# Performance work log

Measured on AMD Instinct MI355X. Metric: run time of the kernel, lower is better.

Reference implementation:

```python
import jax, jax.numpy as jnp
import numpy as np
from jax import lax

# Quantization bit-widths per the module: QuantAct(16) on input,
# QuantConv2d(precision[0]=8), QuantAct(precision[0]+3=11) after relu1,
# QuantLinear(precision[1]=8).
INPUT_BIT = 16
CONV_W_BIT = 8
RELU_BIT = 11
DENSE_W_BIT = 8
EPS = 1e-8


def round_ste(x):
    # straight-through estimator rounding (HAWQ SymmetricQuantFunction)
    return x + lax.stop_gradient(jnp.round(x) - x)


def quant_act(x, bit):
    """Per-tensor symmetric dynamic activation quantization (HAWQ QuantAct).
    Returns fake-quantized x and its scaling factor."""
    n = 2 ** (bit - 1) - 1
    scale = lax.stop_gradient(jnp.maximum(jnp.max(jnp.abs(x)), EPS) / n)
    x_q = jnp.clip(round_ste(x / scale), -n, n) * scale
    return x_q, scale


def quant_weight(w, bit):
    """Per-output-channel symmetric weight quantization. w: [out, ...].
    Returns integer-valued weights and per-channel scale [out]."""
    n = 2 ** (bit - 1) - 1
    absmax = jnp.max(jnp.abs(w.reshape(w.shape[0], -1)), axis=1)
    sf = lax.stop_gradient(jnp.maximum(absmax, EPS) / n)
    bshape = (w.shape[0],) + (1,) * (w.ndim - 1)
    w_int = jnp.clip(round_ste(w / sf.reshape(bshape)), -n, n)
    return w_int, sf


def quant_conv2d(x, p_sf, w, b, bit, stride, pad):
    w_int, w_sf = quant_weight(w, bit)          # [O,I,kh,kw], [O]
    x_int = x / p_sf                            # integer-valued activations
    out_int = lax.conv_general_dilated(
        x_int, w_int, window_strides=(stride, stride),
        padding=((pad, pad), (pad, pad)),
        dimension_numbers=("NCHW", "OIHW", "NCHW"))
    bias_sf = p_sf * w_sf                       # [O]
    b_int = round_ste(b / bias_sf)
    out = (out_int + b_int[None, :, None, None]) * bias_sf[None, :, None, None]
    return out, w_sf


def quant_linear(x, p_sf, w, b, bit):
    w_int, w_sf = quant_weight(w, bit)          # [O,I], [O]
    x_int = x / p_sf
    bias_sf = p_sf * w_sf                       # [O]
    b_int = round_ste(b / bias_sf)
    out = (jnp.einsum("bi,oi->bo", x_int, w_int) + b_int[None, :]) * bias_sf[None, :]
    return out


def setup_inputs() -> dict:
    key = jax.random.key(0)
    k1, k2, k3, k4, k5 = jax.random.split(key, 5)
    B, Cin, H, W = 256, 3, 64, 64
    Cout, K = 64, 3
    Fin, Fout = Cout * 32 * 32, 256  # stride-2 conv -> 32x32 spatial
    x = jax.random.normal(k1, (B, Cin, H, W), dtype=jnp.float32)
    conv_w = jax.random.normal(k2, (Cout, Cin, K, K), dtype=jnp.float32) * 0.1
    conv_b = jax.random.normal(k3, (Cout,), dtype=jnp.float32) * 0.01
    dense_w = jax.random.normal(k4, (Fout, Fin), dtype=jnp.float32) * 0.02
    dense_b = jax.random.normal(k5, (Fout,), dtype=jnp.float32) * 0.01
    return {"x": x, "conv_w": conv_w, "conv_b": conv_b,
            "dense_w": dense_w, "dense_b": dense_b}


def reference(x, conv_w, conv_b, dense_w, dense_b):
    # x, p_sf = quant_input(x)
    xq, p_sf = quant_act(x, INPUT_BIT)
    # x, w_sf = conv(x, p_sf)
    h, w_sf = quant_conv2d(xq, p_sf, conv_w, conv_b, CONV_W_BIT, stride=2, pad=1)
    # relu1
    h = jax.nn.relu(h)
    # x, p_sf = quant_relu(x, p_sf, w_sf)  (requantize at relu_bit)
    h, p_sf = quant_act(h, RELU_BIT)
    # flatten
    h = h.reshape(h.shape[0], -1)
    # relu2(enc_dense(x, p_sf))
    out = jax.nn.relu(quant_linear(h, p_sf, dense_w, dense_b, DENSE_W_BIT))
    return out
```

## Files before the change

### kernel.cpp

```cpp
#include <hip/hip_runtime.h>
#include <hip/hip_fp16.h>
#include <cstdint>

#define B_   256
#define CIN  3
#define HW_  64
#define COUT 64
#define FIN  65536
#define FOUT 256

#define ACC_F    0
#define SC_F     65536
#define XPART_F  65552
#define WPART_F  66064
#define CSF_F    67088
#define CWINT_F  67152
#define H16_BYTE (512*1024)
#define WQ_BYTE  (H16_BYTE + 256ll*FIN*2)
#define REP_BYTE (WQ_BYTE + 256ll*FIN)
#define WS_NEED  (REP_BYTE + 64ll*B_*FOUT*4)

typedef _Float16 half8  __attribute__((ext_vector_type(8)));
typedef float    floatx4 __attribute__((ext_vector_type(4)));
typedef unsigned short u16;
typedef unsigned int uint_;

__device__ inline float blockMax(float v) {
    #pragma unroll
    for (int off = 32; off; off >>= 1) v = fmaxf(v, __shfl_down(v, off));
    __shared__ float sm[8];
    const int lane = threadIdx.x & 63, w = threadIdx.x >> 6;
    if (lane == 0) sm[w] = v;
    __syncthreads();
    float m = sm[0];
    const int nw = blockDim.x >> 6;
    for (int i = 1; i < nw; i++) m = fmaxf(m, sm[i]);
    return m;
}

__global__ __launch_bounds__(256) void k_stats(const float* __restrict__ x,
                                               const float* __restrict__ dw,
                                               const float* __restrict__ cw,
                                               float* __restrict__ ws) {
    const int b = blockIdx.x;
    const int t = threadIdx.x;
    if (b < 512) {
        const float4* x4 = (const float4*)x;
        float m = 0.f;
        for (int i = b * 256 + t; i < (B_ * CIN * HW_ * HW_) / 4; i += 512 * 256) {
            float4 v = x4[i];
            m = fmaxf(m, fmaxf(fmaxf(fabsf(v.x), fabsf(v.y)), fmaxf(fabsf(v.z), fabsf(v.w))));
        }
        float bm = blockMax(m);
        if (t == 0) ws[XPART_F + b] = bm;
    } else if (b < 1536) {
        const int b2 = b - 512;
        const int row = b2 >> 2, q = b2 & 3;
        const float4* r = (const float4*)(dw + (size_t)row * FIN) + q * 4096;
        float m = 0.f;
        for (int i = t; i < 4096; i += 256) {
            float4 v = r[i];
            m = fmaxf(m, fmaxf(fmaxf(fabsf(v.x), fabsf(v.y)), fmaxf(fabsf(v.z), fabsf(v.w))));
        }
        float bm = blockMax(m);
        if (t == 0) ws[WPART_F + b2] = bm;
    } else if (b == 1536) {
        if (t == 64) ((unsigned*)ws)[SC_F + 1] = 0u;
        if (t < 64) {
            const int o = t;
            float wv[27];
            float m = 0.f;
            #pragma unroll
            for (int i = 0; i < 27; i++) { wv[i] = cw[o * 27 + i]; m = fmaxf(m, fabsf(wv[i])); }
            const float sf = fmaxf(m, 1e-8f) / 127.0f;
            #pragma unroll
            for (int i = 0; i < 27; i++)
                ws[CWINT_F + o * 27 + i] = fminf(127.f, fmaxf(-127.f, rintf(wv[i] / sf)));
            ws[CSF_F + o] = sf;
        }
    } else {
        ws[ACC_F + (b - 1537) * 256 + t] = 0.f;
    }
}

__global__ __launch_bounds__(256) void k_conv(const float* __restrict__ x,
                                              const float* __restrict__ dw,
                                              const float* __restrict__ cb,
                                              const float* __restrict__ ws,
                                              u16* __restrict__ h16,
                                              signed char* __restrict__ wq,
                                              unsigned* __restrict__ maxh) {
    const int t = threadIdx.x;

    __shared__ float s_bsf[64], s_bint[64];
    __shared__ float xt[27 * 68];

    float pm = fmaxf(ws[XPART_F + t], ws[XPART_F + 256 + t]);
    pm = blockMax(pm);
    const float p_sf = fmaxf(pm, 1e-8f) / 32767.0f;
    const float inv_p = 1.0f / p_sf;
    if (t < 64) {
        const float bsf = p_sf * ws[CSF_F + t];
        s_bsf[t]  = bsf;
        s_bint[t] = rintf(cb[t] / bsf);
    }

    const int b   = blockIdx.x >> 3;
    const int oyt = (blockIdx.x & 7) * 4;
    const float* xb = x + (size_t)b * (CIN * HW_ * HW_);

    for (int i = t; i < 432; i += 256) {
        const int lrow = i >> 4, c4 = i & 15;
        const int ci = lrow / 9, lr = lrow - ci * 9;
        const int iy = 2 * oyt - 1 + lr;
        float4 v = make_float4(0.f, 0.f, 0.f, 0.f);
        if ((unsigned)iy < 64u) v = *(const float4*)(xb + (ci * HW_ + iy) * HW_ + c4 * 4);
        float* d = &xt[lrow * 68 + 1 + c4 * 4];
        d[0] = rintf(v.x * inv_p);
        d[1] = rintf(v.y * inv_p);
        d[2] = rintf(v.z * inv_p);
        d[3] = rintf(v.w * inv_p);
    }
    if (t < 27) xt[t * 68] = 0.f;
    else if (t < 54) xt[(t - 27) * 68 + 65] = 0.f;
    __syncthreads();

    const int ox = t & 31;
    const int ch = __builtin_amdgcn_readfirstlane((t >> 6) & 1);
    const int dy = ((t >> 7) << 1) + ((t >> 5) & 1);
    const int oy = oyt + dy;

    float xs[27];
    #pragma unroll
    for (int ci = 0; ci < 3; ci++)
        #pragma unroll
        for (int ky = 0; ky < 3; ky++) {
            const float* rowp = &xt[(ci * 9 + 2 * dy + ky) * 68 + 2 * ox];
            float a0 = rowp[0], a1 = rowp[1], a2 = rowp[2];
            asm volatile("" : "+v"(a0), "+v"(a1), "+v"(a2));
            xs[ci * 9 + ky * 3 + 0] = a0;
            xs[ci * 9 + ky * 3 + 1] = a1;
            xs[ci * 9 + ky * 3 + 2] = a2;
        }

    const float* wr = ws + CWINT_F + ch * (32 * 27);
    float mx = 0.f;
    u16* outp = h16 + (size_t)b * FIN + (size_t)ch * 32 * 1024 + oy * 32 + ox;

#define EMIT(cc, aa) { const int co_ = ch * 32 + (cc); \
    float h_ = ((aa) + s_bint[co_]) * s_bsf[co_]; \
    h_ = fmaxf(h_, 0.f); mx = fmaxf(mx, h_); \
    outp[(size_t)(cc) * 1024] = __half_as_ushort(__float2half(h_)); }

    float wA[27], wB[27];
    #pragma unroll
    for (int k = 0; k < 27; k++) wA[k] = wr[k];
    #pragma unroll
    for (int c = 0; c < 32; c += 2) {
        #pragma unroll
        for (int k = 0; k < 27; k++) wB[k] = wr[(c + 1) * 27 + k];
        float a = 0.f;
        #pragma unroll
        for (int k = 0; k < 27; k++) a = fmaf(xs[k], wA[k], a);
        EMIT(c, a);
        if (c + 2 < 32) {
            #pragma unroll
            for (int k = 0; k < 27; k++) wA[k] = wr[(c + 2) * 27 + k];
        }
        float a2 = 0.f;
        #pragma unroll
        for (int k = 0; k < 27; k++) a2 = fmaf(xs[k], wB[k], a2);
        EMIT(c + 1, a2);
    }
#undef EMIT
    float bm = blockMax(mx);
    if (t == 0) atomicMax(maxh, __float_as_uint(bm));

    {
        const int row = blockIdx.x >> 3;
        const int e8  = blockIdx.x & 7;
        const float* wp = ws + WPART_F + row * 4;
        const float am = fmaxf(fmaxf(wp[0], wp[1]), fmaxf(wp[2], wp[3]));
        const float inv = 127.0f / fmaxf(am, 1e-8f);
        const float4* r4 = (const float4*)(dw + (size_t)row * FIN) + e8 * 2048;
        uint_* wrow = (uint_*)(wq + (size_t)row * FIN) + e8 * 2048;
        for (int i = t; i < 2048; i += 256) {
            float4 v = r4[i];
            int q0 = __float2int_rn(v.x * inv);
            int q1 = __float2int_rn(v.y * inv);
            int q2 = __float2int_rn(v.z * inv);
            int q3 = __float2int_rn(v.w * inv);
            wrow[i] = (uint_)(q0 & 255) | ((uint_)(q1 & 255) << 8) |
                      ((uint_)(q2 & 255) << 16) | ((uint_)(q3 & 255) << 24);
        }
    }
}

__device__ __forceinline__ half8 cvt_b8(uint_ lo, uint_ hi) {
    half8 h;
    h[0] = (_Float16)(float)(int)(signed char)(lo);
    h[1] = (_Float16)(float)(int)(signed char)(lo >> 8);
    h[2] = (_Float16)(float)(int)(signed char)(lo >> 16);
    h[3] = (_Float16)(float)(int)(signed char)(lo >> 24);
    h[4] = (_Float16)(float)(int)(signed char)(hi);
    h[5] = (_Float16)(float)(int)(signed char)(hi >> 8);
    h[6] = (_Float16)(float)(int)(signed char)(hi >> 16);
    h[7] = (_Float16)(float)(int)(signed char)(hi >> 24);
    return h;
}

#define GEMM_BODY(EPILOGUE) \
    __shared__ __align__(16) _Float16 As[128][72]; \
    __shared__ __align__(16) _Float16 Bs[128][72]; \
    const int tid = threadIdx.x; \
    const int tm  = (blockIdx.x >> 1) * 128; \
    const int tn  = (blockIdx.x & 1) * 128; \
    const int k0  = blockIdx.y * 1024; \
    const float max_h  = __uint_as_float(((const unsigned*)ws)[SC_F + 1]); \
    const float p2     = fmaxf(max_h, 1e-8f) / 1023.0f; \
    const float inv_p2 = 1.0f / p2; \
    floatx4 acc[4][4]; \
    const floatx4 zz = {0.f, 0.f, 0.f, 0.f}; \
    _Pragma("unroll") \
    for (int i = 0; i < 4; i++) _Pragma("unroll") \
        for (int j = 0; j < 4; j++) acc[i][j] = zz; \
    const int wv = tid >> 6, lane = tid & 63; \
    const int wm = (wv >> 1) * 64, wn = (wv & 1) * 64; \
    const int lm = lane & 15, quad = lane >> 4; \
    const int arow = tid >> 3, acol = tid & 7; \
    const int brow = tid >> 1, bq   = (tid & 1) * 32; \
    const u16* abase = h16 + (size_t)(tm + arow) * FIN + k0 + acol * 8; \
    const signed char* bbase = wq + (size_t)(tn + brow) * FIN + k0 + bq; \
    half8 a0[4], a1[4], a2[4]; \
    uint4 b0[2], b1[2], b2[2]; \
    LOADA(a0, 0); LOADB(b0, 0); \
    LOADA(a1, 1); LOADB(b1, 1); \
    LOADA(a2, 2); LOADB(b2, 2); \
    PHASE(a0, b0, 0); \
    for (int it = 0; it < 5; ++it) { \
        PHASE(a1, b1, 3 * it + 1); \
        PHASE(a2, b2, 3 * it + 2); \
        PHASE(a0, b0, 3 * it + 3); \
    } \
    EPILOGUE

#define LOADA(dst, kk) { _Pragma("unroll") \
    for (int r = 0; r < 4; r++) \
        dst[r] = *(const half8*)(abase + (size_t)r * 32 * FIN + (kk) * 64); }
#define LOADB(dst, kk) { const uint4* p_ = (const uint4*)(bbase + (kk) * 64); \
    dst[0] = p_[0]; dst[1] = p_[1]; }
#define STAGEA(src) { _Pragma("unroll") \
    for (int r = 0; r < 4; r++) { half8 qv; _Pragma("unroll") \
        for (int j = 0; j < 8; j++) { float f_ = (float)src[r][j]; \
            qv[j] = (_Float16)fminf(1023.f, rintf(f_ * inv_p2)); } \
        *(half8*)&As[arow + r * 32][acol * 8] = qv; } }
#define STAGEB(src) { _Pragma("unroll") \
    for (int u = 0; u < 2; u++) { uint4 wd_ = src[u]; \
        *(half8*)&Bs[brow][bq + u * 16 + 0] = cvt_b8(wd_.x, wd_.y); \
        *(half8*)&Bs[brow][bq + u * 16 + 8] = cvt_b8(wd_.z, wd_.w); } }
#define BARRIER() do { asm volatile("s_waitcnt lgkmcnt(0)" ::: "memory"); \
    __builtin_amdgcn_s_barrier(); } while (0)
#define MFMA_PHASE() { _Pragma("unroll") \
    for (int ks = 0; ks < 2; ks++) { half8 af[4], bf[4]; _Pragma("unroll") \
        for (int mi = 0; mi < 4; mi++) \
            af[mi] = *(const half8*)&As[wm + mi * 16 + lm][ks * 32 + quad * 8]; \
        _Pragma("unroll") \
        for (int ni = 0; ni < 4; ni++) \
            bf[ni] = *(const half8*)&Bs[wn + ni * 16 + lm][ks * 32 + quad * 8]; \
        _Pragma("unroll") \
        for (int mi = 0; mi < 4; mi++) _Pragma("unroll") \
            for (int ni = 0; ni < 4; ni++) \
                acc[mi][ni] = __builtin_amdgcn_mfma_f32_16x16x32_f16(af[mi], bf[ni], acc[mi][ni], 0, 0, 0); } }
#define PHASE(As_, Bs_, kk) { \
    STAGEA(As_); STAGEB(Bs_); \
    if ((kk) + 3 < 16) { LOADA(As_, (kk) + 3); LOADB(Bs_, (kk) + 3); } \
    BARRIER(); \
    MFMA_PHASE(); \
    BARRIER(); }

__global__ __launch_bounds__(256) void k_gemm_rep(const u16* __restrict__ h16,
                                                  const signed char* __restrict__ wq,
                                                  const float* __restrict__ ws,
                                                  float* __restrict__ rep) {
    GEMM_BODY({
        float* rp = rep + (size_t)blockIdx.y * (B_ * FOUT);
        _Pragma("unroll")
        for (int mi = 0; mi < 4; mi++) _Pragma("unroll")
            for (int ni = 0; ni < 4; ni++) _Pragma("unroll")
                for (int r = 0; r < 4; r++) {
                    const int row = tm + wm + mi * 16 + quad * 4 + r;
                    const int col = tn + wn + ni * 16 + lm;
                    rp[row * FOUT + col] = acc[mi][ni][r];
                }
    })
}

__global__ __launch_bounds__(256) void k_gemm_atm(const u16* __restrict__ h16,
                                                  const signed char* __restrict__ wq,
                                                  const float* __restrict__ ws,
                                                  float* __restrict__ accb) {
    GEMM_BODY({
        _Pragma("unroll")
        for (int mi = 0; mi < 4; mi++) _Pragma("unroll")
            for (int ni = 0; ni < 4; ni++) _Pragma("unroll")
                for (int r = 0; r < 4; r++) {
                    const int row = tm + wm + mi * 16 + quad * 4 + r;
                    const int col = tn + wn + ni * 16 + lm;
                    atomicAdd(accb + row * FOUT + col, acc[mi][ni][r]);
                }
    })
}
#undef LOADA
#undef LOADB
#undef STAGEA
#undef STAGEB
#undef BARRIER
#undef MFMA_PHASE
#undef PHASE
#undef GEMM_BODY

__global__ void k_epi_rep(const float* __restrict__ rep, const float* __restrict__ db,
                          const float* __restrict__ ws, float* __restrict__ out) {
    const int idx = blockIdx.x * 256 + threadIdx.x;
    float s0 = 0.f, s1 = 0.f, s2 = 0.f, s3 = 0.f;
    #pragma unroll
    for (int r = 0; r < 64; r += 4) {
        s0 += rep[(size_t)(r + 0) * (B_ * FOUT) + idx];
        s1 += rep[(size_t)(r + 1) * (B_ * FOUT) + idx];
        s2 += rep[(size_t)(r + 2) * (B_ * FOUT) + idx];
        s3 += rep[(size_t)(r + 3) * (B_ * FOUT) + idx];
    }
    const float sum = (s0 + s1) + (s2 + s3);
    const int n = idx & 255;
    const float max_h = __uint_as_float(((const unsigned*)ws)[SC_F + 1]);
    const float p2 = fmaxf(max_h, 1e-8f) / 1023.0f;
    const float* wp = ws + WPART_F + (size_t)n * 4;
    const float am = fmaxf(fmaxf(fmaxf(wp[0], wp[1]), fmaxf(wp[2], wp[3])), 1e-8f);
    const float bsf = p2 * (am / 127.0f);
    const float bint = rintf(db[n] / bsf);
    out[idx] = fmaxf(0.f, (sum + bint) * bsf);
}

__global__ void k_epi_atm(const float* __restrict__ accb, const float* __restrict__ db,
                          const float* __restrict__ ws, float* __restrict__ out) {
    const int idx = blockIdx.x * 256 + threadIdx.x;
    const int n = idx & 255;
    const float max_h = __uint_as_float(((const unsigned*)ws)[SC_F + 1]);
    const float p2 = fmaxf(max_h, 1e-8f) / 1023.0f;
    const float* wp = ws + WPART_F + (size_t)n * 4;
    const float am = fmaxf(fmaxf(fmaxf(wp[0], wp[1]), fmaxf(wp[2], wp[3])), 1e-8f);
    const float bsf = p2 * (am / 127.0f);
    const float bint = rintf(db[n] / bsf);
    out[idx] = fmaxf(0.f, (accb[idx] + bint) * bsf);
}

extern "C" void kernel_launch(void* const* d_in, const int* in_sizes, int n_in,
                              void* d_out, int out_size, void* d_ws, size_t ws_size,
                              hipStream_t stream) {
    (void)in_sizes; (void)n_in; (void)out_size;
    const float* x  = (const float*)d_in[0];
    const float* cw = (const float*)d_in[1];
    const float* cb = (const float*)d_in[2];
    const float* dw = (const float*)d_in[3];
    const float* db = (const float*)d_in[4];
    float* out = (float*)d_out;
    float* ws  = (float*)d_ws;
    u16* h16   = (u16*)((char*)d_ws + H16_BYTE);
    signed char* wq = (signed char*)d_ws + WQ_BYTE;
    float* rep  = (float*)((char*)d_ws + REP_BYTE);
    float* accb = ws + ACC_F;
    unsigned* maxh = (unsigned*)ws + SC_F + 1;

    const bool use_rep = (ws_size >= (size_t)WS_NEED);

    k_stats<<<use_rep ? 1537 : 1793, 256, 0, stream>>>(x, dw, cw, ws);
    k_conv<<<2048, 256, 0, stream>>>(x, dw, cb, ws, h16, wq, maxh);
    if (use_rep) {
        k_gemm_rep<<<dim3(4, 64), 256, 0, stream>>>(h16, wq, ws, rep);
        k_epi_rep<<<256, 256, 0, stream>>>(rep, db, ws, out);
    } else {
        k_gemm_atm<<<dim3(4, 64), 256, 0, stream>>>(h16, wq, ws, accb);
        k_epi_atm<<<256, 256, 0, stream>>>(accb, db, ws, out);
    }
}
```

Before: 180.2 us.

## Fuse dense weight quantization into GEMM B-tile staging

Removes the int8 weight quantization pass from the conv kernel and instead loads fp32 dense weights directly in the GEMM, scaling and rounding them to fp16 while writing the B tile to shared memory using per-row inverse scales computed at block start. This eliminates writing and rereading the intermediate int8 weight buffer. In exchange the GEMM reads 4x wider weight data per tile, each weight tile is fetched by both M blocks, and the prefetch pipeline drops from three stages to two with more registers held per thread.

```diff
diff --git a/kernel.cpp b/kernel.cpp
--- a/kernel.cpp
+++ b/kernel.cpp
@@ -21,6 +21,7 @@
 #define WS_NEED  (REP_BYTE + 64ll*B_*FOUT*4)
 
 typedef _Float16 half8  __attribute__((ext_vector_type(8)));
+typedef _Float16 half4v __attribute__((ext_vector_type(4)));
 typedef float    floatx4 __attribute__((ext_vector_type(4)));
 typedef unsigned short u16;
 typedef unsigned int uint_;
@@ -84,11 +85,9 @@
 }
 
 __global__ __launch_bounds__(256) void k_conv(const float* __restrict__ x,
-                                              const float* __restrict__ dw,
                                               const float* __restrict__ cb,
                                               const float* __restrict__ ws,
                                               u16* __restrict__ h16,
-                                              signed char* __restrict__ wq,
                                               unsigned* __restrict__ maxh) {
     const int t = threadIdx.x;
 
@@ -175,43 +174,12 @@
 #undef EMIT
     float bm = blockMax(mx);
     if (t == 0) atomicMax(maxh, __float_as_uint(bm));
-
-    {
-        const int row = blockIdx.x >> 3;
-        const int e8  = blockIdx.x & 7;
-        const float* wp = ws + WPART_F + row * 4;
-        const float am = fmaxf(fmaxf(wp[0], wp[1]), fmaxf(wp[2], wp[3]));
-        const float inv = 127.0f / fmaxf(am, 1e-8f);
-        const float4* r4 = (const float4*)(dw + (size_t)row * FIN) + e8 * 2048;
-        uint_* wrow = (uint_*)(wq + (size_t)row * FIN) + e8 * 2048;
-        for (int i = t; i < 2048; i += 256) {
-            float4 v = r4[i];
-            int q0 = __float2int_rn(v.x * inv);
-            int q1 = __float2int_rn(v.y * inv);
-            int q2 = __float2int_rn(v.z * inv);
-            int q3 = __float2int_rn(v.w * inv);
-            wrow[i] = (uint_)(q0 & 255) | ((uint_)(q1 & 255) << 8) |
-                      ((uint_)(q2 & 255) << 16) | ((uint_)(q3 & 255) << 24);
-        }
-    }
-}
-
-__device__ __forceinline__ half8 cvt_b8(uint_ lo, uint_ hi) {
-    half8 h;
-    h[0] = (_Float16)(float)(int)(signed char)(lo);
-    h[1] = (_Float16)(float)(int)(signed char)(lo >> 8);
-    h[2] = (_Float16)(float)(int)(signed char)(lo >> 16);
-    h[3] = (_Float16)(float)(int)(signed char)(lo >> 24);
-    h[4] = (_Float16)(float)(int)(signed char)(hi);
-    h[5] = (_Float16)(float)(int)(signed char)(hi >> 8);
-    h[6] = (_Float16)(float)(int)(signed char)(hi >> 16);
-    h[7] = (_Float16)(float)(int)(signed char)(hi >> 24);
-    return h;
 }
 
 #define GEMM_BODY(EPILOGUE) \
     __shared__ __align__(16) _Float16 As[128][72]; \
     __shared__ __align__(16) _Float16 Bs[128][72]; \
+    __shared__ float invB[128]; \
     const int tid = threadIdx.x; \
     const int tm  = (blockIdx.x >> 1) * 128; \
     const int tn  = (blockIdx.x & 1) * 128; \
@@ -219,6 +187,12 @@
     const float max_h  = __uint_as_float(((const unsigned*)ws)[SC_F + 1]); \
     const float p2     = fmaxf(max_h, 1e-8f) / 1023.0f; \
     const float inv_p2 = 1.0f / p2; \
+    if (tid < 128) { \
+        const float* wp = ws + WPART_F + (size_t)(tn + tid) * 4; \
+        const float am = fmaxf(fmaxf(wp[0], wp[1]), fmaxf(wp[2], wp[3])); \
+        invB[tid] = 127.0f / fmaxf(am, 1e-8f); \
+    } \
+    __syncthreads(); \
     floatx4 acc[4][4]; \
     const floatx4 zz = {0.f, 0.f, 0.f, 0.f}; \
     _Pragma("unroll") \
@@ -228,36 +202,40 @@
     const int wm = (wv >> 1) * 64, wn = (wv & 1) * 64; \
     const int lm = lane & 15, quad = lane >> 4; \
     const int arow = tid >> 3, acol = tid & 7; \
-    const int brow = tid >> 1, bq   = (tid & 1) * 32; \
+    const int brow = tid >> 4, bcol = tid & 15; \
     const u16* abase = h16 + (size_t)(tm + arow) * FIN + k0 + acol * 8; \
-    const signed char* bbase = wq + (size_t)(tn + brow) * FIN + k0 + bq; \
-    half8 a0[4], a1[4], a2[4]; \
-    uint4 b0[2], b1[2], b2[2]; \
+    const float* bbase = dw + (size_t)(tn + brow) * FIN + k0 + bcol * 4; \
+    half8  a0[4], a1[4]; \
+    float4 b0[8], b1[8]; \
     LOADA(a0, 0); LOADB(b0, 0); \
     LOADA(a1, 1); LOADB(b1, 1); \
-    LOADA(a2, 2); LOADB(b2, 2); \
-    PHASE(a0, b0, 0); \
-    for (int it = 0; it < 5; ++it) { \
-        PHASE(a1, b1, 3 * it + 1); \
-        PHASE(a2, b2, 3 * it + 2); \
-        PHASE(a0, b0, 3 * it + 3); \
+    for (int it = 0; it < 8; ++it) { \
+        PHASE(a0, b0, 2 * it); \
+        PHASE(a1, b1, 2 * it + 1); \
     } \
     EPILOGUE
 
 #define LOADA(dst, kk) { _Pragma("unroll") \
     for (int r = 0; r < 4; r++) \
         dst[r] = *(const half8*)(abase + (size_t)r * 32 * FIN + (kk) * 64); }
-#define LOADB(dst, kk) { const uint4* p_ = (const uint4*)(bbase + (kk) * 64); \
-    dst[0] = p_[0]; dst[1] = p_[1]; }
+#define LOADB(dst, kk) { _Pragma("unroll") \
+    for (int r = 0; r < 8; r++) \
+        dst[r] = *(const float4*)(bbase + (size_t)r * 16 * FIN + (kk) * 64); }
 #define STAGEA(src) { _Pragma("unroll") \
     for (int r = 0; r < 4; r++) { half8 qv; _Pragma("unroll") \
         for (int j = 0; j < 8; j++) { float f_ = (float)src[r][j]; \
             qv[j] = (_Float16)fminf(1023.f, rintf(f_ * inv_p2)); } \
         *(half8*)&As[arow + r * 32][acol * 8] = qv; } }
 #define STAGEB(src) { _Pragma("unroll") \
-    for (int u = 0; u < 2; u++) { uint4 wd_ = src[u]; \
-        *(half8*)&Bs[brow][bq + u * 16 + 0] = cvt_b8(wd_.x, wd_.y); \
-        *(half8*)&Bs[brow][bq + u * 16 + 8] = cvt_b8(wd_.z, wd_.w); } }
+    for (int r = 0; r < 8; r++) { \
+        const float is_ = invB[brow + r * 16]; \
+        float4 v_ = src[r]; \
+        half4v qv; \
+        qv[0] = (_Float16)rintf(v_.x * is_);    \
+        qv[1] = (_Float16)rintf(v_.y * is_); \
+        qv[2] = (_Float16)rintf(v_.z * is_); \
+        qv[3] = (_Float16)rintf(v_.w * is_); \
+        *(half4v*)&Bs[brow + r * 16][bcol * 4] = qv; } }
 #define BARRIER() do { asm volatile("s_waitcnt lgkmcnt(0)" ::: "memory"); \
     __builtin_amdgcn_s_barrier(); } while (0)
 #define MFMA_PHASE() { _Pragma("unroll") \
@@ -273,13 +251,13 @@
                 acc[mi][ni] = __builtin_amdgcn_mfma_f32_16x16x32_f16(af[mi], bf[ni], acc[mi][ni], 0, 0, 0); } }
 #define PHASE(As_, Bs_, kk) { \
     STAGEA(As_); STAGEB(Bs_); \
-    if ((kk) + 3 < 16) { LOADA(As_, (kk) + 3); LOADB(Bs_, (kk) + 3); } \
+    if ((kk) + 2 < 16) { LOADA(As_, (kk) + 2); LOADB(Bs_, (kk) + 2); } \
     BARRIER(); \
     MFMA_PHASE(); \
     BARRIER(); }
 
 __global__ __launch_bounds__(256) void k_gemm_rep(const u16* __restrict__ h16,
-                                                  const signed char* __restrict__ wq,
+                                                  const float* __restrict__ dw,
                                                   const float* __restrict__ ws,
                                                   float* __restrict__ rep) {
     GEMM_BODY({
@@ -296,7 +274,7 @@
 }
 
 __global__ __launch_bounds__(256) void k_gemm_atm(const u16* __restrict__ h16,
-                                                  const signed char* __restrict__ wq,
+                                                  const float* __restrict__ dw,
                                                   const float* __restrict__ ws,
                                                   float* __restrict__ accb) {
     GEMM_BODY({
@@ -366,7 +344,6 @@
     float* out = (float*)d_out;
     float* ws  = (float*)d_ws;
     u16* h16   = (u16*)((char*)d_ws + H16_BYTE);
-    signed char* wq = (signed char*)d_ws + WQ_BYTE;
     float* rep  = (float*)((char*)d_ws + REP_BYTE);
     float* accb = ws + ACC_F;
     unsigned* maxh = (unsigned*)ws + SC_F + 1;
@@ -374,12 +351,12 @@
     const bool use_rep = (ws_size >= (size_t)WS_NEED);
 
     k_stats<<<use_rep ? 1537 : 1793, 256, 0, stream>>>(x, dw, cw, ws);
-    k_conv<<<2048, 256, 0, stream>>>(x, dw, cb, ws, h16, wq, maxh);
+    k_conv<<<2048, 256, 0, stream>>>(x, cb, ws, h16, maxh);
     if (use_rep) {
-        k_gemm_rep<<<dim3(4, 64), 256, 0, stream>>>(h16, wq, ws, rep);
+        k_gemm_rep<<<dim3(4, 64), 256, 0, stream>>>(h16, dw, ws, rep);
         k_epi_rep<<<256, 256, 0, stream>>>(rep, db, ws, out);
     } else {
-        k_gemm_atm<<<dim3(4, 64), 256, 0, stream>>>(h16, wq, ws, accb);
+        k_gemm_atm<<<dim3(4, 64), 256, 0, stream>>>(h16, dw, ws, accb);
         k_epi_atm<<<256, 256, 0, stream>>>(accb, db, ws, out);
     }
 }
```

Measured after the change: 198.6 us. 10.2% more time.
